# Optimization experiments

Measured on AMD Instinct MI355X. Metric: run time of the kernel, lower is better.

Reference implementation:

```python
import jax, jax.numpy as jnp
import numpy as np

TOPK, NUM_CLASSES, ALPHA, BETA = 13, 80, 1.0, 6.0
IOU_EPS = 1e-7


def _cxcywh_to_xyxy(b):
    cx, cy, w, h = b[..., 0], b[..., 1], b[..., 2], b[..., 3]
    return cx - w / 2, cy - h / 2, cx + w / 2, cy + h / 2


def _pairwise_iou(pd, gt):
    # pd: [B,A,4] cxcywh, gt: [B,G,4] cxcywh -> iou [B,A,G]
    p1x, p1y, p2x, p2y = _cxcywh_to_xyxy(pd)
    g1x, g1y, g2x, g2y = _cxcywh_to_xyxy(gt)
    ix1 = jnp.maximum(p1x[:, :, None], g1x[:, None, :])
    iy1 = jnp.maximum(p1y[:, :, None], g1y[:, None, :])
    ix2 = jnp.minimum(p2x[:, :, None], g2x[:, None, :])
    iy2 = jnp.minimum(p2y[:, :, None], g2y[:, None, :])
    inter = jnp.clip(ix2 - ix1, 0) * jnp.clip(iy2 - iy1, 0)
    area_p = (p2x - p1x) * (p2y - p1y)  # [B,A]
    area_g = (g2x - g1x) * (g2y - g1y)  # [B,G]
    union = area_p[:, :, None] + area_g[:, None, :] - inter + IOU_EPS
    return inter / union


def setup_inputs() -> dict:
    key = jax.random.key(0)
    ks = jax.random.split(key, 8)
    B, A, G, C = 32, 8400, 64, 80
    img = 640.0
    pd_scores = jax.random.normal(ks[0], (B, A, C), dtype=jnp.float32)
    pd_cxy = jax.random.uniform(ks[1], (B, A, 2)) * img
    pd_wh = jax.random.uniform(ks[2], (B, A, 2)) * 115.0 + 5.0
    pd_bboxes = jnp.concatenate([pd_cxy, pd_wh], axis=-1).astype(jnp.float32)
    anc_points = (jax.random.uniform(ks[3], (A, 2)) * img).astype(jnp.float32)
    gt_labels = jax.random.randint(ks[4], (B, G, 1), 0, C, dtype=jnp.int32)
    gt_cxy = jax.random.uniform(ks[5], (B, G, 2)) * img
    gt_wh = jax.random.uniform(ks[6], (B, G, 2)) * 115.0 + 5.0
    gt_bboxes = jnp.concatenate([gt_cxy, gt_wh], axis=-1).astype(jnp.float32)
    mask_gt = jax.random.uniform(ks[7], (B, G, 1)) < 0.7  # bool
    return {"pd_scores": pd_scores, "pd_bboxes": pd_bboxes, "anc_points": anc_points,
            "gt_labels": gt_labels, "gt_bboxes": gt_bboxes, "mask_gt": mask_gt}


def reference(pd_scores, pd_bboxes, anc_points, gt_labels, gt_bboxes, mask_gt):
    B, A, C = pd_scores.shape
    G = gt_bboxes.shape[1]
    valid = mask_gt[..., 0].astype(bool)          # [B,G]
    labels = gt_labels[..., 0].astype(jnp.int32)  # [B,G]

    overlaps = _pairwise_iou(pd_bboxes, gt_bboxes)                 # [B,A,G]
    onehot_gt = jax.nn.one_hot(labels, C, dtype=pd_scores.dtype)   # [B,G,C]
    score_gt = jnp.einsum('bac,bgc->bag', pd_scores, onehot_gt)    # gather score at gt class
    metrics = jax.nn.sigmoid(score_gt) ** ALPHA * overlaps ** BETA  # [B,A,G], >= 0
    metrics = jnp.where(valid[:, None, :], metrics, -1.0)          # invalid gt -> sentinel

    # top-k anchors per gt (dim over anchors)
    _, topk_idx = jax.lax.top_k(jnp.swapaxes(metrics, 1, 2), TOPK)  # [B,G,k]
    b_ix = jnp.arange(B)[:, None, None]
    g_ix = jnp.arange(G)[None, :, None]
    cand = jnp.zeros((B, A, G), dtype=bool).at[b_ix, topk_idx, g_ix].set(True)
    cand = cand & valid[:, None, :]

    # (last such gt under ties, matching sequential overwrite order);
    # otherwise the first candidate gt keeps the anchor.
    anchor_max = metrics.max(axis=-1)                               # [B,A]
    is_max_cand = (metrics >= anchor_max[..., None]) & cand         # [B,A,G]
    has_max = is_max_cand.any(axis=-1)
    last_max = (G - 1) - jnp.argmax(is_max_cand[:, :, ::-1].astype(jnp.int32), axis=-1)
    first_cand = jnp.argmax(cand.astype(jnp.int32), axis=-1)
    assigned = jnp.where(has_max, last_max, first_cand)             # [B,A]
    fg = cand.any(axis=-1)                                          # [B,A] bool

    asg_label = jnp.take_along_axis(labels, assigned, axis=1)                   # [B,A]
    asg_bbox = jnp.take_along_axis(gt_bboxes, assigned[:, :, None], axis=1)     # [B,A,4]
    asg_iou = jnp.take_along_axis(overlaps, assigned[:, :, None], axis=2)[..., 0]  # [B,A]

    oh = jax.nn.one_hot(asg_label, C, dtype=pd_scores.dtype)
    fgf = fg.astype(pd_scores.dtype)
    target_labels = oh * fgf[..., None]
    target_bboxes = asg_bbox * fgf[..., None]
    target_scores = oh * (asg_iou * fgf)[..., None]
    return target_labels, target_bboxes, target_scores, fg
```

## Files before the change

### kernel.cpp

```cpp
#include <hip/hip_runtime.h>

#define NB 32
#define NA 8400
#define NG 64
#define NC 80
#define NK 13
#define TILE0 64
#define NT0 132

#define OFF_LBL  0
#define OFF_BBOX 21504000
#define OFF_SCR  22579200
#define OFF_FG   44083200

#define WS_METRICS_SZ  (32ull*64*8400*4)
#define WS_MASK_SZ     (32ull*8400*8)
#define WS_AMAX_SZ     (32ull*8400*4)
#define WS_NEEDED      (WS_METRICS_SZ + WS_MASK_SZ + WS_AMAX_SZ)

__device__ __forceinline__ float sigmoid_f(float x) {
    return 1.0f / (1.0f + expf(-x));
}

__device__ __forceinline__ float iou_corners(
    float px1, float py1, float px2, float py2, float ap,
    float gx1, float gy1, float gx2, float gy2, float ag)
{
    float ix1 = fmaxf(px1, gx1), iy1 = fmaxf(py1, gy1);
    float ix2 = fminf(px2, gx2), iy2 = fminf(py2, gy2);
    float inter = fmaxf(ix2 - ix1, 0.0f) * fmaxf(iy2 - iy1, 0.0f);
    return inter / (ap + ag - inter + 1e-7f);
}

__global__ __launch_bounds__(256) void metrics_kernel(
    const float* __restrict__ pd_scores,
    const float* __restrict__ pd_bboxes,
    const int* __restrict__ gt_labels,
    const float* __restrict__ gt_bboxes,
    const int* __restrict__ mask_gt,
    float* __restrict__ metrics,
    float* __restrict__ amax_arr,
    unsigned long long* __restrict__ cmask)
{
    const int b  = blockIdx.y;
    const int a0 = blockIdx.x * TILE0;
    const int tid = threadIdx.x;
    const int an = min(TILE0, NA - a0);

    __shared__ float s_sc[TILE0 * 81];
    __shared__ float s_pb[TILE0 * 5];
    __shared__ float s_gb[NG * 5];
    __shared__ float s_pm[4][TILE0];
    __shared__ int   s_lab[NG];
    __shared__ int   s_val[NG];

    const float* sbase = pd_scores + ((size_t)b * NA + a0) * NC;
    for (int i4 = tid; i4 < an * 20; i4 += 256) {
        const float4 v = reinterpret_cast<const float4*>(sbase)[i4];
        const int al = i4 / 20;
        const int c  = (i4 % 20) * 4;
        float* d = &s_sc[al * 81 + c];
        d[0] = sigmoid_f(v.x); d[1] = sigmoid_f(v.y);
        d[2] = sigmoid_f(v.z); d[3] = sigmoid_f(v.w);
    }
    if (tid < an) {
        const float4 pb = *reinterpret_cast<const float4*>(pd_bboxes + ((size_t)b * NA + a0 + tid) * 4);
        const float px1 = pb.x - pb.z * 0.5f, py1 = pb.y - pb.w * 0.5f;
        const float px2 = pb.x + pb.z * 0.5f, py2 = pb.y + pb.w * 0.5f;
        s_pb[tid * 5 + 0] = px1; s_pb[tid * 5 + 1] = py1;
        s_pb[tid * 5 + 2] = px2; s_pb[tid * 5 + 3] = py2;
        s_pb[tid * 5 + 4] = (px2 - px1) * (py2 - py1);
    }
    if (tid >= 64 && tid < 64 + NG) {
        const int g = tid - 64;
        const float4 gb = *reinterpret_cast<const float4*>(gt_bboxes + ((size_t)b * NG + g) * 4);
        const float gx1 = gb.x - gb.z * 0.5f, gy1 = gb.y - gb.w * 0.5f;
        const float gx2 = gb.x + gb.z * 0.5f, gy2 = gb.y + gb.w * 0.5f;
        s_gb[g * 5 + 0] = gx1; s_gb[g * 5 + 1] = gy1;
        s_gb[g * 5 + 2] = gx2; s_gb[g * 5 + 3] = gy2;
        s_gb[g * 5 + 4] = (gx2 - gx1) * (gy2 - gy1);
        s_lab[g] = gt_labels[b * NG + g];
        s_val[g] = mask_gt[b * NG + g];
    }
    __syncthreads();

    const int a_local = tid & 63;
    const int ggrp    = tid >> 6;
    float pm = -1.0f;
    if (a_local < an) {
        const float px1 = s_pb[a_local * 5 + 0], py1 = s_pb[a_local * 5 + 1];
        const float px2 = s_pb[a_local * 5 + 2], py2 = s_pb[a_local * 5 + 3];
        const float ap  = s_pb[a_local * 5 + 4];
        #pragma unroll 4
        for (int gg = 0; gg < 16; ++gg) {
            const int g = gg * 4 + ggrp;
            float m = -1.0f;
            if (s_val[g]) {
                const float iou = iou_corners(px1, py1, px2, py2, ap,
                                              s_gb[g*5+0], s_gb[g*5+1], s_gb[g*5+2], s_gb[g*5+3], s_gb[g*5+4]);
                const float i2 = iou * iou;
                m = s_sc[a_local * 81 + s_lab[g]] * (i2 * i2 * i2);
            }
            pm = fmaxf(pm, m);
            metrics[((size_t)(b * NG + g)) * NA + a0 + a_local] = m;
        }
    }
    s_pm[ggrp][a_local] = pm;
    __syncthreads();
    if (tid < an) {
        const float am = fmaxf(fmaxf(s_pm[0][tid], s_pm[1][tid]),
                               fmaxf(s_pm[2][tid], s_pm[3][tid]));
        amax_arr[(size_t)b * NA + a0 + tid] = am;
        cmask[(size_t)b * NA + a0 + tid] = 0ull;
    }
}

__global__ __launch_bounds__(256) void topk_kernel(
    const float* __restrict__ metrics,
    const int* __restrict__ mask_gt,
    unsigned long long* __restrict__ cand_mask)
{
    const int g = blockIdx.x;
    const int b = blockIdx.y;
    const int tid = threadIdx.x;

    if (mask_gt[b * NG + g] == 0) return;

    const float* __restrict__ mrow = metrics + (size_t)(b * NG + g) * NA;

    float v[NK]; int ix[NK];
    #pragma unroll
    for (int k = 0; k < NK; ++k) { v[k] = -3.0f; ix[k] = 0x7fffffff; }

    for (int base = tid * 4; base < NA; base += 1024) {
        const float4 m4 = *reinterpret_cast<const float4*>(mrow + base);
        const float mv4[4] = {m4.x, m4.y, m4.z, m4.w};
        #pragma unroll
        for (int j = 0; j < 4; ++j) {
            float m = mv4[j];
            int   a = base + j;
            if (m > v[NK-1]) {
                #pragma unroll
                for (int k = 0; k < NK; ++k) {
                    if (m > v[k]) {
                        const float tv = v[k]; v[k] = m;  m = tv;
                        const int   ti = ix[k]; ix[k] = a; a = ti;
                    }
                }
            }
        }
    }

    __shared__ float s_wv[4];
    __shared__ int   s_wi[4];
    __shared__ int   s_sel[NK];

    for (int r = 0; r < NK; ++r) {
        float bv = v[0]; int bi = ix[0];
        #pragma unroll
        for (int off = 32; off; off >>= 1) {
            const float ov = __shfl_xor(bv, off);
            const int   oi = __shfl_xor(bi, off);
            if (ov > bv || (ov == bv && oi < bi)) { bv = ov; bi = oi; }
        }
        if ((tid & 63) == 0) { s_wv[tid >> 6] = bv; s_wi[tid >> 6] = bi; }
        __syncthreads();
        bv = s_wv[0]; bi = s_wi[0];
        #pragma unroll
        for (int w = 1; w < 4; ++w) {
            if (s_wv[w] > bv || (s_wv[w] == bv && s_wi[w] < bi)) { bv = s_wv[w]; bi = s_wi[w]; }
        }
        if (tid == 0) s_sel[r] = bi;
        if (v[0] == bv && ix[0] == bi) {
            #pragma unroll
            for (int k = 0; k < NK - 1; ++k) { v[k] = v[k+1]; ix[k] = ix[k+1]; }
            v[NK-1] = -3.0f; ix[NK-1] = 0x7fffffff;
        }
        __syncthreads();
    }

    if (tid < NK) {
        atomicOr(&cand_mask[(size_t)b * NA + s_sel[tid]], 1ull << g);
    }
}

__global__ __launch_bounds__(256) void assign_kernel(
    const float* __restrict__ metrics,
    const float* __restrict__ amax_arr,
    const float* __restrict__ pd_bboxes,
    const int* __restrict__ gt_labels,
    const float* __restrict__ gt_bboxes,
    const unsigned long long* __restrict__ cand_mask,
    float* __restrict__ out)
{
    const int b = blockIdx.y;
    const int a0 = blockIdx.x * 256;
    const int tid = threadIdx.x;
    const int a = a0 + tid;
    const bool active = a < NA;

    __shared__ float s_gb[NG * 5];
    __shared__ float s_graw[NG][4];
    __shared__ int   s_lab[NG];
    __shared__ int   s_albl[256];
    __shared__ float s_aiou[256];

    if (tid < NG) {
        const float4 gb = *reinterpret_cast<const float4*>(gt_bboxes + ((size_t)b * NG + tid) * 4);
        s_graw[tid][0] = gb.x; s_graw[tid][1] = gb.y; s_graw[tid][2] = gb.z; s_graw[tid][3] = gb.w;
        const float gx1 = gb.x - gb.z * 0.5f, gy1 = gb.y - gb.w * 0.5f;
        const float gx2 = gb.x + gb.z * 0.5f, gy2 = gb.y + gb.w * 0.5f;
        s_gb[tid * 5 + 0] = gx1; s_gb[tid * 5 + 1] = gy1;
        s_gb[tid * 5 + 2] = gx2; s_gb[tid * 5 + 3] = gy2;
        s_gb[tid * 5 + 4] = (gx2 - gx1) * (gy2 - gy1);
        s_lab[tid] = gt_labels[b * NG + tid];
    }
    __syncthreads();

    unsigned long long cand = 0ull;
    if (active) cand = cand_mask[(size_t)b * NA + a];
    const bool fg = (cand != 0ull);

    int assigned = 0;
    float aiou = 0.0f;
    if (fg) {
        const float am = amax_arr[(size_t)b * NA + a];
        const int first = __ffsll(cand) - 1;
        int last = -1;
        unsigned long long rem = cand;
        while (rem) {
            const int g = __ffsll(rem) - 1;
            rem &= rem - 1;
            const float mv = metrics[((size_t)(b * NG + g)) * NA + a];
            if (mv >= am) last = g;
        }
        assigned = (last >= 0) ? last : first;
        const float4 pb = *reinterpret_cast<const float4*>(pd_bboxes + ((size_t)b * NA + a) * 4);
        const float px1 = pb.x - pb.z * 0.5f, py1 = pb.y - pb.w * 0.5f;
        const float px2 = pb.x + pb.z * 0.5f, py2 = pb.y + pb.w * 0.5f;
        const float ap = (px2 - px1) * (py2 - py1);
        aiou = iou_corners(px1, py1, px2, py2, ap,
                           s_gb[assigned*5+0], s_gb[assigned*5+1],
                           s_gb[assigned*5+2], s_gb[assigned*5+3], s_gb[assigned*5+4]);
    }

    s_albl[tid] = fg ? s_lab[assigned] : -1;
    s_aiou[tid] = fg ? aiou : 0.0f;

    if (active) {
        float4 ob = fg ? make_float4(s_graw[assigned][0], s_graw[assigned][1],
                                     s_graw[assigned][2], s_graw[assigned][3])
                       : make_float4(0.f, 0.f, 0.f, 0.f);
        *reinterpret_cast<float4*>(out + OFF_BBOX + ((size_t)b * NA + a) * 4) = ob;
        out[OFF_FG + (size_t)b * NA + a] = fg ? 1.0f : 0.0f;
    }
    __syncthreads();

    const int cnt = min(256, NA - a0);
    float4* __restrict__ lblp = reinterpret_cast<float4*>(out + OFF_LBL + ((size_t)b * NA + a0) * NC);
    float4* __restrict__ scrp = reinterpret_cast<float4*>(out + OFF_SCR + ((size_t)b * NA + a0) * NC);
    for (int i4 = tid; i4 < cnt * 20; i4 += 256) {
        const int al = i4 / 20;
        const int cb = (i4 - al * 20) * 4;
        const int lbl = s_albl[al];
        const float aio = s_aiou[al];
        float4 l4, s4;
        l4.x = (cb + 0 == lbl) ? 1.0f : 0.0f;  s4.x = (cb + 0 == lbl) ? aio : 0.0f;
        l4.y = (cb + 1 == lbl) ? 1.0f : 0.0f;  s4.y = (cb + 1 == lbl) ? aio : 0.0f;
        l4.z = (cb + 2 == lbl) ? 1.0f : 0.0f;  s4.z = (cb + 2 == lbl) ? aio : 0.0f;
        l4.w = (cb + 3 == lbl) ? 1.0f : 0.0f;  s4.w = (cb + 3 == lbl) ? aio : 0.0f;
        lblp[i4] = l4;
        scrp[i4] = s4;
    }
}

__global__ __launch_bounds__(256) void topk_fb(
    const float* __restrict__ pd_scores, const float* __restrict__ pd_bboxes,
    const int* __restrict__ gt_labels, const float* __restrict__ gt_bboxes,
    const int* __restrict__ mask_gt, int* __restrict__ topk_idx)
{
    const int g = blockIdx.x, b = blockIdx.y, tid = threadIdx.x;
    int* outp = topk_idx + (b * NG + g) * NK;
    if (mask_gt[b * NG + g] == 0) { if (tid < NK) outp[tid] = -1; return; }
    __shared__ float sm[NA];
    __shared__ float wv[4]; __shared__ int wi[4];
    const int label = gt_labels[b * NG + g];
    const float4 gb = *reinterpret_cast<const float4*>(gt_bboxes + (size_t)(b * NG + g) * 4);
    const float gx1 = gb.x - gb.z * 0.5f, gy1 = gb.y - gb.w * 0.5f;
    const float gx2 = gb.x + gb.z * 0.5f, gy2 = gb.y + gb.w * 0.5f;
    const float ag = (gx2 - gx1) * (gy2 - gy1);
    for (int a = tid; a < NA; a += 256) {
        const float4 pb = *reinterpret_cast<const float4*>(pd_bboxes + ((size_t)b * NA + a) * 4);
        const float px1 = pb.x - pb.z * 0.5f, py1 = pb.y - pb.w * 0.5f;
        const float px2 = pb.x + pb.z * 0.5f, py2 = pb.y + pb.w * 0.5f;
        const float ap = (px2 - px1) * (py2 - py1);
        const float iou = iou_corners(px1, py1, px2, py2, ap, gx1, gy1, gx2, gy2, ag);
        const float s = pd_scores[((size_t)b * NA + a) * NC + label];
        const float i2 = iou * iou;
        sm[a] = sigmoid_f(s) * (i2 * i2 * i2);
    }
    __syncthreads();
    for (int k = 0; k < NK; ++k) {
        float bv = -3.0f; int bi = 0x7fffffff;
        for (int a = tid; a < NA; a += 256) {
            const float vv = sm[a];
            if (vv > bv || (vv == bv && a < bi)) { bv = vv; bi = a; }
        }
        #pragma unroll
        for (int off = 32; off; off >>= 1) {
            const float ov = __shfl_xor(bv, off); const int oi = __shfl_xor(bi, off);
            if (ov > bv || (ov == bv && oi < bi)) { bv = ov; bi = oi; }
        }
        if ((tid & 63) == 0) { wv[tid >> 6] = bv; wi[tid >> 6] = bi; }
        __syncthreads();
        if (tid == 0) {
            #pragma unroll
            for (int w = 1; w < 4; ++w)
                if (wv[w] > bv || (wv[w] == bv && wi[w] < bi)) { bv = wv[w]; bi = wi[w]; }
            outp[k] = bi; sm[bi] = -2.0f;
        }
        __syncthreads();
    }
}

__global__ __launch_bounds__(256) void assign_fb(
    const float* __restrict__ pd_scores, const float* __restrict__ pd_bboxes,
    const int* __restrict__ gt_labels, const float* __restrict__ gt_bboxes,
    const int* __restrict__ mask_gt, const int* __restrict__ topk_idx,
    float* __restrict__ out)
{
    const int b = blockIdx.y, a0 = blockIdx.x * 256, tid = threadIdx.x;
    __shared__ float s_gx1[NG], s_gy1[NG], s_gx2[NG], s_gy2[NG], s_gar[NG];
    __shared__ float s_graw[NG][4];
    __shared__ int s_lab[NG], s_val[NG], s_tk[NG][NK], s_albl[256];
    __shared__ float s_aiou[256];
    if (tid < NG) {
        const float4 gb = *reinterpret_cast<const float4*>(gt_bboxes + ((size_t)b * NG + tid) * 4);
        s_graw[tid][0] = gb.x; s_graw[tid][1] = gb.y; s_graw[tid][2] = gb.z; s_graw[tid][3] = gb.w;
        const float gx1 = gb.x - gb.z * 0.5f, gy1 = gb.y - gb.w * 0.5f;
        const float gx2 = gb.x + gb.z * 0.5f, gy2 = gb.y + gb.w * 0.5f;
        s_gx1[tid] = gx1; s_gy1[tid] = gy1; s_gx2[tid] = gx2; s_gy2[tid] = gy2;
        s_gar[tid] = (gx2 - gx1) * (gy2 - gy1);
        s_lab[tid] = gt_labels[b * NG + tid];
        s_val[tid] = mask_gt[b * NG + tid];
    }
    for (int i = tid; i < NG * NK; i += 256) s_tk[i / NK][i % NK] = topk_idx[(size_t)b * NG * NK + i];
    __syncthreads();
    const int a = a0 + tid;
    const bool active = a < NA;
    float anchor_max = -1.0f;
    unsigned long long cand = 0ull;
    float px1 = 0, py1 = 0, px2 = 0, py2 = 0, ap = 0;
    const float* srow = pd_scores + ((size_t)b * NA + a) * NC;
    if (active) {
        const float4 pb = *reinterpret_cast<const float4*>(pd_bboxes + ((size_t)b * NA + a) * 4);
        px1 = pb.x - pb.z * 0.5f; py1 = pb.y - pb.w * 0.5f;
        px2 = pb.x + pb.z * 0.5f; py2 = pb.y + pb.w * 0.5f;
        ap = (px2 - px1) * (py2 - py1);
        for (int g = 0; g < NG; ++g) {
            if (!s_val[g]) continue;
            const float iou = iou_corners(px1, py1, px2, py2, ap, s_gx1[g], s_gy1[g], s_gx2[g], s_gy2[g], s_gar[g]);
            const float i2 = iou * iou;
            const float m = sigmoid_f(srow[s_lab[g]]) * (i2 * i2 * i2);
            anchor_max = fmaxf(anchor_max, m);
            bool c = false;
            #pragma unroll
            for (int k = 0; k < NK; ++k) c = c || (s_tk[g][k] == a);
            if (c) cand |= (1ull << g);
        }
    }
    const bool fg = (cand != 0ull);
    int assigned = 0; float aiou = 0.0f;
    if (fg) {
        const int first = __ffsll(cand) - 1;
        int lastg = -1;
        unsigned long long rem = cand;
        while (rem) {
            const int g = __ffsll(rem) - 1; rem &= rem - 1;
            const float iou = iou_corners(px1, py1, px2, py2, ap, s_gx1[g], s_gy1[g], s_gx2[g], s_gy2[g], s_gar[g]);
            const float i2 = iou * iou;
            const float m = sigmoid_f(srow[s_lab[g]]) * (i2 * i2 * i2);
            if (m >= anchor_max) lastg = g;
        }
        assigned = (lastg >= 0) ? lastg : first;
        aiou = iou_corners(px1, py1, px2, py2, ap, s_gx1[assigned], s_gy1[assigned], s_gx2[assigned], s_gy2[assigned], s_gar[assigned]);
    }
    s_albl[tid] = fg ? s_lab[assigned] : -1;
    s_aiou[tid] = fg ? aiou : 0.0f;
    if (active) {
        float4 ob = fg ? make_float4(s_graw[assigned][0], s_graw[assigned][1], s_graw[assigned][2], s_graw[assigned][3])
                       : make_float4(0.f, 0.f, 0.f, 0.f);
        *reinterpret_cast<float4*>(out + OFF_BBOX + ((size_t)b * NA + a) * 4) = ob;
        out[OFF_FG + (size_t)b * NA + a] = fg ? 1.0f : 0.0f;
    }
    __syncthreads();
    const int cnt = min(256, NA - a0);
    for (int i = tid; i < cnt * NC; i += 256) {
        const int al = i / NC, c = i - al * NC;
        const int lbl = s_albl[al];
        const size_t base = ((size_t)b * NA + (a0 + al)) * NC + c;
        out[OFF_LBL + base] = (c == lbl) ? 1.0f : 0.0f;
        out[OFF_SCR + base] = (c == lbl) ? s_aiou[al] : 0.0f;
    }
}

extern "C" void kernel_launch(void* const* d_in, const int* in_sizes, int n_in,
                              void* d_out, int out_size, void* d_ws, size_t ws_size,
                              hipStream_t stream) {
    const float* pd_scores = (const float*)d_in[0];
    const float* pd_bboxes = (const float*)d_in[1];
    const int*   gt_labels = (const int*)d_in[3];
    const float* gt_bboxes = (const float*)d_in[4];
    const int*   mask_gt   = (const int*)d_in[5];
    float* out = (float*)d_out;

    if (ws_size >= WS_NEEDED) {
        float* metrics = (float*)d_ws;
        unsigned long long* cmask = (unsigned long long*)((char*)d_ws + WS_METRICS_SZ);
        float* amax_arr = (float*)((char*)d_ws + WS_METRICS_SZ + WS_MASK_SZ);

        dim3 g0(NT0, NB);
        metrics_kernel<<<g0, 256, 0, stream>>>(pd_scores, pd_bboxes, gt_labels, gt_bboxes,
                                               mask_gt, metrics, amax_arr, cmask);

        dim3 g1(NG, NB);
        topk_kernel<<<g1, 256, 0, stream>>>(metrics, mask_gt, cmask);

        dim3 g2((NA + 255) / 256, NB);
        assign_kernel<<<g2, 256, 0, stream>>>(metrics, amax_arr, pd_bboxes, gt_labels, gt_bboxes,
                                              cmask, out);
    } else {
        int* topk = (int*)d_ws;
        dim3 g1(NG, NB);
        topk_fb<<<g1, 256, 0, stream>>>(pd_scores, pd_bboxes, gt_labels, gt_bboxes, mask_gt, topk);
        dim3 g2((NA + 255) / 256, NB);
        assign_fb<<<g2, 256, 0, stream>>>(pd_scores, pd_bboxes, gt_labels, gt_bboxes, mask_gt, topk, out);
    }
}
```

Before: 367.8 us.

## Replace full metrics matrix with per-tile top-k partials and precomputed max bits

The metrics kernel no longer writes the full B×G×A metric matrix. Each wavefront ranks its 64 anchors per gt with ballot and shuffle and writes only the top-13 (value, index) pairs per tile into a partials buffer. The merge kernel reduces these 132×13 candidates per gt instead of scanning 8400 values. It also marks which selected anchors reach the per-anchor maximum, so the assign kernel no longer re-reads metrics to pick the assigned gt. This removes a large amount of global write and read traffic, in exchange for an O(n) shuffle ranking loop per gt in the metrics kernel. Partial slots are only partly filled when a tile has fewer than 13 non-negative entries, which leaves stale workspace entries in the merge input and risks wrong results.

```diff
diff --git a/kernel.cpp b/kernel.cpp
--- a/kernel.cpp
+++ b/kernel.cpp
@@ -13,10 +13,11 @@
 #define OFF_SCR  22579200
 #define OFF_FG   44083200
 
-#define WS_METRICS_SZ  (32ull*64*8400*4)
-#define WS_MASK_SZ     (32ull*8400*8)
-#define WS_AMAX_SZ     (32ull*8400*4)
-#define WS_NEEDED      (WS_METRICS_SZ + WS_MASK_SZ + WS_AMAX_SZ)
+#define WS_PART_SZ  (32ull*64*132*13*8)
+#define WS_MASK_SZ  (32ull*8400*8)
+#define WS_AMAX_SZ  (32ull*8400*4)
+#define WS_MAXB_SZ  (32ull*8400*8)
+#define WS_NEEDED   (WS_PART_SZ + WS_MASK_SZ + WS_AMAX_SZ + WS_MAXB_SZ)
 
 __device__ __forceinline__ float sigmoid_f(float x) {
     return 1.0f / (1.0f + expf(-x));
@@ -38,14 +39,16 @@
     const int* __restrict__ gt_labels,
     const float* __restrict__ gt_bboxes,
     const int* __restrict__ mask_gt,
-    float* __restrict__ metrics,
+    float2* __restrict__ partials,
     float* __restrict__ amax_arr,
-    unsigned long long* __restrict__ cmask)
-{
-    const int b  = blockIdx.y;
-    const int a0 = blockIdx.x * TILE0;
+    unsigned long long* __restrict__ cmask,
+    unsigned long long* __restrict__ maxbits)
+{
+    const int b   = blockIdx.y;
+    const int til = blockIdx.x;
+    const int a0  = til * TILE0;
     const int tid = threadIdx.x;
-    const int an = min(TILE0, NA - a0);
+    const int an  = min(TILE0, NA - a0);
 
     __shared__ float s_sc[TILE0 * 81];
     __shared__ float s_pb[TILE0 * 5];
@@ -63,10 +66,13 @@
         d[0] = sigmoid_f(v.x); d[1] = sigmoid_f(v.y);
         d[2] = sigmoid_f(v.z); d[3] = sigmoid_f(v.w);
     }
-    if (tid < an) {
-        const float4 pb = *reinterpret_cast<const float4*>(pd_bboxes + ((size_t)b * NA + a0 + tid) * 4);
-        const float px1 = pb.x - pb.z * 0.5f, py1 = pb.y - pb.w * 0.5f;
-        const float px2 = pb.x + pb.z * 0.5f, py2 = pb.y + pb.w * 0.5f;
+    if (tid < TILE0) {
+        float px1 = 0, py1 = 0, px2 = 0, py2 = 0;
+        if (tid < an) {
+            const float4 pb = *reinterpret_cast<const float4*>(pd_bboxes + ((size_t)b * NA + a0 + tid) * 4);
+            px1 = pb.x - pb.z * 0.5f; py1 = pb.y - pb.w * 0.5f;
+            px2 = pb.x + pb.z * 0.5f; py2 = pb.y + pb.w * 0.5f;
+        }
         s_pb[tid * 5 + 0] = px1; s_pb[tid * 5 + 1] = py1;
         s_pb[tid * 5 + 2] = px2; s_pb[tid * 5 + 3] = py2;
         s_pb[tid * 5 + 4] = (px2 - px1) * (py2 - py1);
@@ -84,41 +90,66 @@
     }
     __syncthreads();
 
-    const int a_local = tid & 63;
-    const int ggrp    = tid >> 6;
+    const int lane = tid & 63;
+    const int wgrp = tid >> 6;
+    const float px1 = s_pb[lane * 5 + 0], py1 = s_pb[lane * 5 + 1];
+    const float px2 = s_pb[lane * 5 + 2], py2 = s_pb[lane * 5 + 3];
+    const float ap  = s_pb[lane * 5 + 4];
     float pm = -1.0f;
-    if (a_local < an) {
-        const float px1 = s_pb[a_local * 5 + 0], py1 = s_pb[a_local * 5 + 1];
-        const float px2 = s_pb[a_local * 5 + 2], py2 = s_pb[a_local * 5 + 3];
-        const float ap  = s_pb[a_local * 5 + 4];
-        #pragma unroll 4
-        for (int gg = 0; gg < 16; ++gg) {
-            const int g = gg * 4 + ggrp;
-            float m = -1.0f;
-            if (s_val[g]) {
-                const float iou = iou_corners(px1, py1, px2, py2, ap,
-                                              s_gb[g*5+0], s_gb[g*5+1], s_gb[g*5+2], s_gb[g*5+3], s_gb[g*5+4]);
-                const float i2 = iou * iou;
-                m = s_sc[a_local * 81 + s_lab[g]] * (i2 * i2 * i2);
+
+    #pragma unroll 4
+    for (int gg = 0; gg < 16; ++gg) {
+        const int g = gg * 4 + wgrp;
+        float m = -1.0f;
+        if (lane < an && s_val[g]) {
+            const float iou = iou_corners(px1, py1, px2, py2, ap,
+                                          s_gb[g*5+0], s_gb[g*5+1], s_gb[g*5+2], s_gb[g*5+3], s_gb[g*5+4]);
+            const float i2 = iou * iou;
+            m = s_sc[lane * 81 + s_lab[g]] * (i2 * i2 * i2);
+        }
+        pm = fmaxf(pm, m);
+
+        const unsigned long long pos = __ballot(m > 0.0f);
+        const unsigned long long zer = __ballot(m == 0.0f);
+        const int n = __popcll(pos);
+        int slot = -1;
+        if (m > 0.0f) {
+            int r = 0;
+            unsigned long long rem = pos;
+            while (rem) {
+                const int j = __ffsll(rem) - 1;
+                rem &= rem - 1;
+                const float vj = __shfl(m, j);
+                r += (vj > m || (vj == m && j < lane)) ? 1 : 0;
             }
-            pm = fmaxf(pm, m);
-            metrics[((size_t)(b * NG + g)) * NA + a0 + a_local] = m;
-        }
-    }
-    s_pm[ggrp][a_local] = pm;
+            if (r < NK) slot = r;
+        } else if (m == 0.0f && n < NK) {
+            const int p = __popcll(zer & ((1ull << lane) - 1ull));
+            if (p < NK - n) slot = n + p;
+        }
+        if (slot >= 0) {
+            float2 e; e.x = m; e.y = __int_as_float(a0 + lane);
+            partials[(((size_t)(b * NG + g)) * NT0 + til) * NK + slot] = e;
+        }
+    }
+
+    s_pm[wgrp][lane] = pm;
     __syncthreads();
     if (tid < an) {
         const float am = fmaxf(fmaxf(s_pm[0][tid], s_pm[1][tid]),
                                fmaxf(s_pm[2][tid], s_pm[3][tid]));
         amax_arr[(size_t)b * NA + a0 + tid] = am;
-        cmask[(size_t)b * NA + a0 + tid] = 0ull;
-    }
-}
-
-__global__ __launch_bounds__(256) void topk_kernel(
-    const float* __restrict__ metrics,
+        cmask[(size_t)b * NA + a0 + tid]   = 0ull;
+        maxbits[(size_t)b * NA + a0 + tid] = 0ull;
+    }
+}
+
+__global__ __launch_bounds__(256) void merge_kernel(
+    const float2* __restrict__ partials,
+    const float* __restrict__ amax_arr,
     const int* __restrict__ mask_gt,
-    unsigned long long* __restrict__ cand_mask)
+    unsigned long long* __restrict__ cmask,
+    unsigned long long* __restrict__ maxbits)
 {
     const int g = blockIdx.x;
     const int b = blockIdx.y;
@@ -126,26 +157,22 @@
 
     if (mask_gt[b * NG + g] == 0) return;
 
-    const float* __restrict__ mrow = metrics + (size_t)(b * NG + g) * NA;
+    const float2* __restrict__ row = partials + ((size_t)(b * NG + g)) * NT0 * NK;
 
     float v[NK]; int ix[NK];
     #pragma unroll
     for (int k = 0; k < NK; ++k) { v[k] = -3.0f; ix[k] = 0x7fffffff; }
 
-    for (int base = tid * 4; base < NA; base += 1024) {
-        const float4 m4 = *reinterpret_cast<const float4*>(mrow + base);
-        const float mv4[4] = {m4.x, m4.y, m4.z, m4.w};
-        #pragma unroll
-        for (int j = 0; j < 4; ++j) {
-            float m = mv4[j];
-            int   a = base + j;
-            if (m > v[NK-1]) {
-                #pragma unroll
-                for (int k = 0; k < NK; ++k) {
-                    if (m > v[k]) {
-                        const float tv = v[k]; v[k] = m;  m = tv;
-                        const int   ti = ix[k]; ix[k] = a; a = ti;
-                    }
+    for (int i = tid; i < NT0 * NK; i += 256) {
+        const float2 e = row[i];
+        float m = e.x;
+        int   a = __float_as_int(e.y);
+        if (m > v[NK-1]) {
+            #pragma unroll
+            for (int k = 0; k < NK; ++k) {
+                if (m > v[k]) {
+                    const float tv = v[k]; v[k] = m;  m = tv;
+                    const int   ti = ix[k]; ix[k] = a; a = ti;
                 }
             }
         }
@@ -154,6 +181,7 @@
     __shared__ float s_wv[4];
     __shared__ int   s_wi[4];
     __shared__ int   s_sel[NK];
+    __shared__ float s_selv[NK];
 
     for (int r = 0; r < NK; ++r) {
         float bv = v[0]; int bi = ix[0];
@@ -170,7 +198,7 @@
         for (int w = 1; w < 4; ++w) {
             if (s_wv[w] > bv || (s_wv[w] == bv && s_wi[w] < bi)) { bv = s_wv[w]; bi = s_wi[w]; }
         }
-        if (tid == 0) s_sel[r] = bi;
+        if (tid == 0) { s_sel[r] = bi; s_selv[r] = bv; }
         if (v[0] == bv && ix[0] == bi) {
             #pragma unroll
             for (int k = 0; k < NK - 1; ++k) { v[k] = v[k+1]; ix[k] = ix[k+1]; }
@@ -180,17 +208,20 @@
     }
 
     if (tid < NK) {
-        atomicOr(&cand_mask[(size_t)b * NA + s_sel[tid]], 1ull << g);
+        const int a = s_sel[tid];
+        atomicOr(&cmask[(size_t)b * NA + a], 1ull << g);
+        if (s_selv[tid] >= amax_arr[(size_t)b * NA + a]) {
+            atomicOr(&maxbits[(size_t)b * NA + a], 1ull << g);
+        }
     }
 }
 
 __global__ __launch_bounds__(256) void assign_kernel(
-    const float* __restrict__ metrics,
-    const float* __restrict__ amax_arr,
     const float* __restrict__ pd_bboxes,
     const int* __restrict__ gt_labels,
     const float* __restrict__ gt_bboxes,
-    const unsigned long long* __restrict__ cand_mask,
+    const unsigned long long* __restrict__ cmask,
+    const unsigned long long* __restrict__ maxbits,
     float* __restrict__ out)
 {
     const int b = blockIdx.y;
@@ -217,24 +248,17 @@
     }
     __syncthreads();
 
-    unsigned long long cand = 0ull;
-    if (active) cand = cand_mask[(size_t)b * NA + a];
+    unsigned long long cand = 0ull, maxb = 0ull;
+    if (active) {
+        cand = cmask[(size_t)b * NA + a];
+        maxb = maxbits[(size_t)b * NA + a];
+    }
     const bool fg = (cand != 0ull);
 
     int assigned = 0;
     float aiou = 0.0f;
     if (fg) {
-        const float am = amax_arr[(size_t)b * NA + a];
-        const int first = __ffsll(cand) - 1;
-        int last = -1;
-        unsigned long long rem = cand;
-        while (rem) {
-            const int g = __ffsll(rem) - 1;
-            rem &= rem - 1;
-            const float mv = metrics[((size_t)(b * NG + g)) * NA + a];
-            if (mv >= am) last = g;
-        }
-        assigned = (last >= 0) ? last : first;
+        assigned = maxb ? (63 - __clzll(maxb)) : (__ffsll(cand) - 1);
         const float4 pb = *reinterpret_cast<const float4*>(pd_bboxes + ((size_t)b * NA + a) * 4);
         const float px1 = pb.x - pb.z * 0.5f, py1 = pb.y - pb.w * 0.5f;
         const float px2 = pb.x + pb.z * 0.5f, py2 = pb.y + pb.w * 0.5f;
@@ -415,20 +439,20 @@
     float* out = (float*)d_out;
 
     if (ws_size >= WS_NEEDED) {
-        float* metrics = (float*)d_ws;
-        unsigned long long* cmask = (unsigned long long*)((char*)d_ws + WS_METRICS_SZ);
-        float* amax_arr = (float*)((char*)d_ws + WS_METRICS_SZ + WS_MASK_SZ);
+        float2* partials = (float2*)d_ws;
+        unsigned long long* cmask = (unsigned long long*)((char*)d_ws + WS_PART_SZ);
+        float* amax_arr = (float*)((char*)d_ws + WS_PART_SZ + WS_MASK_SZ);
+        unsigned long long* maxbits = (unsigned long long*)((char*)d_ws + WS_PART_SZ + WS_MASK_SZ + WS_AMAX_SZ);
 
         dim3 g0(NT0, NB);
         metrics_kernel<<<g0, 256, 0, stream>>>(pd_scores, pd_bboxes, gt_labels, gt_bboxes,
-                                               mask_gt, metrics, amax_arr, cmask);
+                                               mask_gt, partials, amax_arr, cmask, maxbits);
 
         dim3 g1(NG, NB);
-        topk_kernel<<<g1, 256, 0, stream>>>(metrics, mask_gt, cmask);
+        merge_kernel<<<g1, 256, 0, stream>>>(partials, amax_arr, mask_gt, cmask, maxbits);
 
         dim3 g2((NA + 255) / 256, NB);
-        assign_kernel<<<g2, 256, 0, stream>>>(metrics, amax_arr, pd_bboxes, gt_labels, gt_bboxes,
-                                              cmask, out);
+        assign_kernel<<<g2, 256, 0, stream>>>(pd_bboxes, gt_labels, gt_bboxes, cmask, maxbits, out);
     } else {
         int* topk = (int*)d_ws;
         dim3 g1(NG, NB);
```

Result: faster. 322.6 us (-12.3%).
